# Kernel tuning notes

Measured on AMD Instinct MI355X. Metric: run time of the kernel, lower is better.

## Reference

```python
import jax, jax.numpy as jnp
import numpy as np

B, S, D, H = 32, 577, 768, 12
DH = D // H
MLP = 4 * D
EPS = 1e-5


def _layernorm(x, g, b):
    m = jnp.mean(x, axis=-1, keepdims=True)
    v = jnp.mean((x - m) ** 2, axis=-1, keepdims=True)
    return (x - m) * jax.lax.rsqrt(v + EPS) * g + b


def setup_inputs() -> dict:
    key = jax.random.key(0)
    ks = jax.random.split(key, 12)
    w = lambda k, shp: (jax.random.normal(k, shp, dtype=jnp.float32) * 0.02)
    return {
        "x": jax.random.normal(ks[0], (B, S, D), dtype=jnp.float32),
        "ln1_g": jnp.ones((D,), jnp.float32), "ln1_b": jnp.zeros((D,), jnp.float32),
        "ln2_g": jnp.ones((D,), jnp.float32), "ln2_b": jnp.zeros((D,), jnp.float32),
        "wq": w(ks[1], (H, DH, DH)), "bq": jnp.zeros((H, DH), jnp.float32),
        "wk": w(ks[2], (H, DH, DH)), "bk": jnp.zeros((H, DH), jnp.float32),
        "wv": w(ks[3], (H, DH, DH)), "bv": jnp.zeros((H, DH), jnp.float32),
        "w1": w(ks[4], (D, MLP)), "b1": jnp.zeros((MLP,), jnp.float32),
        "w2": w(ks[5], (MLP, D)), "b2": jnp.zeros((D,), jnp.float32),
    }


def reference(x, ln1_g, ln1_b, ln2_g, ln2_b, wq, bq, wk, bk, wv, bv, w1, b1, w2, b2):
    b, s, d = x.shape
    xn = _layernorm(x, ln1_g, ln1_b)
    xh = xn.reshape(b, s, H, DH)  # split heads along last dim (as in torch slicing)
    # per-head linear maps, batched over heads: [B,H,S,DH]
    q = jnp.einsum('bshd,hdo->bhso', xh, wq) + bq[:, None, :]
    k = jnp.einsum('bshd,hdo->bhso', xh, wk) + bk[:, None, :]
    v = jnp.einsum('bshd,hdo->bhso', xh, wv) + bv[:, None, :]
    scores = jnp.einsum('bhso,bhto->bhst', q, k) / (DH ** 0.5)
    attn = jax.nn.softmax(scores, axis=-1)  # softmax over keys (torch dim=1 of [S,S])
    o = jnp.einsum('bhst,bhtd->bshd', attn, v).reshape(b, s, d)
    out = x + o
    yn = _layernorm(out, ln2_g, ln2_b)
    h = jax.nn.gelu(yn @ w1 + b1, approximate=False)  # torch GELU default is erf-based
    return out + h @ w2 + b2
```

## Files before the change

kernel.cpp:

```cpp
#include <hip/hip_runtime.h>

#define S_LEN 577
#define SPAD  640
#define DMODEL 768
#define NH 12
#define DHEAD 64
#define MLPD 3072
#define NROWS (32 * 577)
#define MPAD  18688
#define NBH   (32 * 12)
#define LOG2E 1.44269504088896340736f

typedef __attribute__((ext_vector_type(8))) short s8v;
typedef __attribute__((ext_vector_type(4))) float f4v;

#define MFMA16(a, b, c) __builtin_amdgcn_mfma_f32_16x16x32_bf16((a), (b), (c), 0, 0, 0)

__device__ __forceinline__ short f2bf(float f) {
  union { float f; unsigned u; } a; a.f = f;
  unsigned r = a.u + 0x7FFFu + ((a.u >> 16) & 1u);
  return (short)(r >> 16);
}
__device__ __forceinline__ short f2bfF(float f) {
  union { float f; unsigned u; } a; a.f = f;
  return (short)((a.u + 0x8000u) >> 16);
}

__device__ __forceinline__ void gload16(const short* g, const short* l) {
  __builtin_amdgcn_global_load_lds(
      (const __attribute__((address_space(1))) void*)g,
      (__attribute__((address_space(3))) void*)l, 16, 0, 0);
}

__global__ __launch_bounds__(256) void transpose_w(const float* __restrict__ in,
                                                   short* __restrict__ out, int R, int C) {
  __shared__ float tile[32][33];
  int c0 = blockIdx.x * 32, r0 = blockIdx.y * 32;
  int tx = threadIdx.x, ty = threadIdx.y;
  for (int i = ty; i < 32; i += 8) tile[i][tx] = in[(size_t)(r0 + i) * C + c0 + tx];
  __syncthreads();
  for (int i = ty; i < 32; i += 8) out[(size_t)(c0 + i) * R + r0 + tx] = f2bf(tile[tx][i]);
}

__global__ __launch_bounds__(256) void prep_qkv(const float* __restrict__ wq, const float* __restrict__ wk,
                                                const float* __restrict__ wv, short* __restrict__ oq,
                                                short* __restrict__ ok, short* __restrict__ ov) {
  int h = blockIdx.x, t = threadIdx.x;
  const float* src0 = wq + (size_t)h * 4096;
  const float* src1 = wk + (size_t)h * 4096;
  const float* src2 = wv + (size_t)h * 4096;
  short* dst0 = oq + (size_t)h * 4096;
  short* dst1 = ok + (size_t)h * 4096;
  short* dst2 = ov + (size_t)h * 4096;
  for (int i = t; i < 4096; i += 256) {
    int o = i >> 6, d = i & 63;
    dst0[i] = f2bf(src0[d * 64 + o]);
    dst1[i] = f2bf(src1[d * 64 + o]);
    dst2[i] = f2bf(src2[d * 64 + o]);
  }
}

__global__ __launch_bounds__(256) void pad_kv(short* __restrict__ kg, short* __restrict__ vt) {
  int idx = blockIdx.x * 256 + threadIdx.x;
  const int padw = SPAD - S_LEN;
  const int per = DHEAD * padw;
  if (idx >= NBH * per) return;
  int bh = idx / per, r = idx - bh * per;
  int col = r / padw, s = S_LEN + (r - col * padw);
  vt[((size_t)bh * DHEAD + col) * SPAD + s] = 0;
  kg[((size_t)bh * SPAD + s) * DHEAD + col] = 0;
}

__global__ __launch_bounds__(256) void ln_kernel(const float* __restrict__ x, const float* __restrict__ g,
                                                 const float* __restrict__ bta, short* __restrict__ out) {
  int row = blockIdx.x;
  int t = threadIdx.x;
  const float* xr = x + (size_t)row * DMODEL;
  float v0 = xr[t], v1 = xr[t + 256], v2 = xr[t + 512];
  float s = v0 + v1 + v2;
  float s2 = v0 * v0 + v1 * v1 + v2 * v2;
  for (int o = 32; o; o >>= 1) { s += __shfl_down(s, o); s2 += __shfl_down(s2, o); }
  __shared__ float red[8];
  if ((t & 63) == 0) { int w = t >> 6; red[w] = s; red[4 + w] = s2; }
  __syncthreads();
  s = red[0] + red[1] + red[2] + red[3];
  s2 = red[4] + red[5] + red[6] + red[7];
  float m = s * (1.f / DMODEL);
  float rs = rsqrtf(s2 * (1.f / DMODEL) - m * m + 1e-5f);
  short* orow = out + (size_t)row * DMODEL;
  orow[t]       = f2bf((v0 - m) * rs * g[t]       + bta[t]);
  orow[t + 256] = f2bf((v1 - m) * rs * g[t + 256] + bta[t + 256]);
  orow[t + 512] = f2bf((v2 - m) * rs * g[t + 512] + bta[t + 512]);
}

__global__ __launch_bounds__(256) void qkv_kernel(const short* __restrict__ xn,
    const short* __restrict__ wqt, const short* __restrict__ wkt, const short* __restrict__ wvt,
    const float* __restrict__ bq, const float* __restrict__ bk, const float* __restrict__ bv,
    short* __restrict__ qg, short* __restrict__ kg, short* __restrict__ vt) {
  __shared__ __align__(16) short wl[3][64][72];
  int bid = blockIdx.x;
  int h = bid % NH, mt = bid / NH;
  int t = threadIdx.x;
  {
    int o = t >> 2, d0 = (t & 3) * 16;
    const short* s0 = wqt + (size_t)h * 4096 + o * 64 + d0;
    const short* s1 = wkt + (size_t)h * 4096 + o * 64 + d0;
    const short* s2 = wvt + (size_t)h * 4096 + o * 64 + d0;
    *(uint4*)&wl[0][o][d0]     = *(const uint4*)s0;
    *(uint4*)&wl[0][o][d0 + 8] = *(const uint4*)(s0 + 8);
    *(uint4*)&wl[1][o][d0]     = *(const uint4*)s1;
    *(uint4*)&wl[1][o][d0 + 8] = *(const uint4*)(s1 + 8);
    *(uint4*)&wl[2][o][d0]     = *(const uint4*)s2;
    *(uint4*)&wl[2][o][d0 + 8] = *(const uint4*)(s2 + 8);
  }
  __syncthreads();
  int w = t >> 6, l = t & 63, l15 = l & 15, lh = l >> 4;
  int m0 = mt * 64 + w * 16;
  if (m0 >= NROWS) return;
  f4v z = {0.f, 0.f, 0.f, 0.f};
  f4v aq[4], ak[4], av[4];
#pragma unroll
  for (int nt = 0; nt < 4; ++nt) { aq[nt] = z; ak[nt] = z; av[nt] = z; }
  const short* xrow = xn + (size_t)(m0 + l15) * DMODEL + h * DHEAD;
#pragma unroll
  for (int kk = 0; kk < 64; kk += 32) {
    s8v af = *(const s8v*)(xrow + kk + lh * 8);
#pragma unroll
    for (int nt = 0; nt < 4; ++nt) {
      s8v b0 = *(const s8v*)&wl[0][nt * 16 + l15][kk + lh * 8];
      s8v b1 = *(const s8v*)&wl[1][nt * 16 + l15][kk + lh * 8];
      s8v b2 = *(const s8v*)&wl[2][nt * 16 + l15][kk + lh * 8];
      aq[nt] = MFMA16(af, b0, aq[nt]);
      ak[nt] = MFMA16(af, b1, ak[nt]);
      av[nt] = MFMA16(af, b2, av[nt]);
    }
  }
#pragma unroll
  for (int nt = 0; nt < 4; ++nt) {
    int col = nt * 16 + l15;
    float biq = bq[h * DHEAD + col], bik = bk[h * DHEAD + col], biv = bv[h * DHEAD + col];
#pragma unroll
    for (int i = 0; i < 4; ++i) {
      int m = m0 + lh * 4 + i;
      int bb = m / S_LEN;
      int ss = m - bb * S_LEN;
      int bh = bb * NH + h;
      qg[((size_t)bh * S_LEN + ss) * DHEAD + col] = f2bf((aq[nt][i] + biq) * (0.125f * LOG2E));
      kg[((size_t)bh * SPAD + ss) * DHEAD + col]  = f2bf(ak[nt][i] + bik);
      vt[((size_t)bh * DHEAD + col) * SPAD + ss]  = f2bf(av[nt][i] + biv);
    }
  }
}

__global__ __launch_bounds__(64, 2) void attn_kernel(const short* __restrict__ qg, const short* __restrict__ kg,
                                                     const short* __restrict__ vt, const float* __restrict__ x,
                                                     float* __restrict__ outp) {
  __shared__ __align__(16) short Pb[2][64][72];
  int bh = blockIdx.x;
  int qt = blockIdx.y;
  int h = bh % NH, b = bh / NH;
  int l = threadIdx.x & 63, l15 = l & 15, lh = l >> 4;
  int q0 = qt * 64;
  size_t qbase = (size_t)bh * S_LEN * DHEAD;
  size_t kbase = (size_t)bh * SPAD * DHEAD;
  size_t vbase = (size_t)bh * DHEAD * SPAD;
  s8v aq[4][2];
#pragma unroll
  for (int f = 0; f < 4; ++f) {
    int qrow = q0 + f * 16 + l15; if (qrow > 576) qrow = 576;
    const short* qp = qg + qbase + (size_t)qrow * DHEAD + lh * 8;
    aq[f][0] = *(const s8v*)qp;
    aq[f][1] = *(const s8v*)(qp + 32);
  }
  f4v z = {0.f, 0.f, 0.f, 0.f};
  f4v z16 = {-16.f, -16.f, -16.f, -16.f};
  f4v acc[4][4];
  float lsum[4][4];
#pragma unroll
  for (int f = 0; f < 4; ++f) {
#pragma unroll
    for (int dt = 0; dt < 4; ++dt) acc[f][dt] = z;
#pragma unroll
    for (int i = 0; i < 4; ++i) lsum[f][i] = 0.f;
  }

  s8v kf0[4], kf1[4], vf[2][4];
  f4v sc[2][4];

#define LOADK(KB)                                                      \
  {                                                                    \
    _Pragma("unroll")                                                  \
    for (int nt = 0; nt < 4; ++nt) {                                   \
      const short* kp = kg + kbase + (size_t)((KB) + nt * 16 + l15) * DHEAD + lh * 8; \
      kf0[nt] = *(const s8v*)kp;                                       \
      kf1[nt] = *(const s8v*)(kp + 32);                                \
    }                                                                  \
  }

#define LOADV(KB)                                                      \
  {                                                                    \
    _Pragma("unroll")                                                  \
    for (int kk2 = 0; kk2 < 2; ++kk2) {                                \
      const short* vp = vt + vbase + (KB) + kk2 * 32 + lh * 8;         \
      _Pragma("unroll")                                                \
      for (int dt = 0; dt < 4; ++dt)                                   \
        vf[kk2][dt] = *(const s8v*)(vp + (size_t)(dt * 16 + l15) * SPAD); \
    }                                                                  \
  }

#define QKT_H(FH)                                                      \
  {                                                                    \
    __builtin_amdgcn_s_setprio(1);                                     \
    _Pragma("unroll")                                                  \
    for (int nt = 0; nt < 4; ++nt) {                                   \
      _Pragma("unroll")                                                \
      for (int fo = 0; fo < 2; ++fo) {                                 \
        f4v a = MFMA16(aq[2 * (FH) + fo][0], kf0[nt], z16);            \
        a = MFMA16(aq[2 * (FH) + fo][1], kf1[nt], a);                  \
        sc[fo][nt] = a;                                                \
      }                                                                \
    }                                                                  \
    __builtin_amdgcn_s_setprio(0);                                     \
  }

#define SMAX_H(FH, PAR, MASK)                                          \
  {                                                                    \
    if (MASK) {                                                        \
      _Pragma("unroll")                                                \
      for (int nt = 0; nt < 4; ++nt) {                                 \
        int col = 576 + nt * 16 + l15;                                 \
        if (col > 576) {                                               \
          _Pragma("unroll")                                            \
          for (int fo = 0; fo < 2; ++fo) {                             \
            sc[fo][nt][0] = sc[fo][nt][1] = sc[fo][nt][2] = sc[fo][nt][3] = -1e30f; } \
        }                                                              \
      }                                                                \
    }                                                                  \
    _Pragma("unroll")                                                  \
    for (int fo = 0; fo < 2; ++fo)                                     \
      _Pragma("unroll")                                                \
      for (int i = 0; i < 4; ++i) {                                    \
        float s = lsum[2 * (FH) + fo][i];                              \
        _Pragma("unroll")                                              \
        for (int nt = 0; nt < 4; ++nt) {                               \
          float e = exp2f(sc[fo][nt][i]);                              \
          s += e;                                                      \
          Pb[PAR][(2 * (FH) + fo) * 16 + lh * 4 + i][nt * 16 + l15] = f2bfF(e); \
        }                                                              \
        lsum[2 * (FH) + fo][i] = s;                                    \
      }                                                                \
  }

#define PVT(PAR)                                                       \
  {                                                                    \
    __builtin_amdgcn_s_setprio(1);                                     \
    _Pragma("unroll")                                                  \
    for (int kk2 = 0; kk2 < 2; ++kk2) {                                \
      _Pragma("unroll")                                                \
      for (int f = 0; f < 4; ++f) {                                    \
        s8v af = *(const s8v*)&Pb[PAR][f * 16 + l15][kk2 * 32 + lh * 8]; \
        _Pragma("unroll")                                              \
        for (int dt = 0; dt < 4; ++dt)                                 \
          acc[f][dt] = MFMA16(af, vf[kk2][dt], acc[f][dt]);            \
      }                                                                \
    }                                                                  \
    __builtin_amdgcn_s_setprio(0);                                     \
  }

  LOADK(0);
  QKT_H(0);
  SMAX_H(0, 0, false);
  QKT_H(1);
  LOADK(64);
  SMAX_H(1, 0, false);

  for (int kt = 0; kt < 10; ++kt) {
    int par = kt & 1;
    LOADV(kt * 64);
    if (kt < 9) {
      bool mask = (kt == 8);
      QKT_H(0);
      SMAX_H(0, par ^ 1, mask);
      QKT_H(1);
      if (kt < 8) LOADK((kt + 2) * 64);
      SMAX_H(1, par ^ 1, mask);
    }
    PVT(par);
  }
#undef LOADK
#undef LOADV
#undef QKT_H
#undef SMAX_H
#undef PVT
#pragma unroll
  for (int f = 0; f < 4; ++f)
#pragma unroll
    for (int i = 0; i < 4; ++i) {
      float s = lsum[f][i];
      s += __shfl_xor(s, 1);
      s += __shfl_xor(s, 2);
      s += __shfl_xor(s, 4);
      s += __shfl_xor(s, 8);
      int srow = q0 + f * 16 + lh * 4 + i;
      if (srow > 576) continue;
      float inv = __builtin_amdgcn_rcpf(s);
      size_t idx0 = ((size_t)b * S_LEN + srow) * DMODEL + h * DHEAD + l15;
#pragma unroll
      for (int dt = 0; dt < 4; ++dt) {
        size_t idx = idx0 + dt * 16;
        outp[idx] = x[idx] + acc[f][dt][i] * inv;
      }
    }
}

#define BARR asm volatile("s_barrier" ::: "memory")

#define STAGE_HALF(G, SH, bufi, half, ktile)                                       \
  do {                                                                             \
    _Pragma("unroll") for (int rd = 0; rd < 2; ++rd) {                             \
      int rw_ = rd * 64 + (tid >> 3);                                              \
      int sl_ = (tid & 7) ^ (rw_ & 7);                                             \
      gload16((G) + (size_t)((half) * 128 + rw_) * K + (ktile) * 64 + sl_ * 8,     \
              &SH[bufi][(half) * 128 + rw_][(tid & 7) * 8]);                       \
    }                                                                              \
  } while (0)

#define READ_A(rh)                                                                 \
  _Pragma("unroll") for (int mt = 0; mt < 4; ++mt)                                 \
    _Pragma("unroll") for (int kh = 0; kh < 2; ++kh)                               \
      af[mt][kh] = *(const s8v*)&sA[cur][(rh) * 128 + wr * 64 + mt * 16 + l15]     \
                                    [((kh * 4 + lh) ^ s7) * 8];

#define READ_B(BF, chh)                                                            \
  _Pragma("unroll") for (int nt = 0; nt < 2; ++nt)                                 \
    _Pragma("unroll") for (int kh = 0; kh < 2; ++kh)                               \
      BF[nt][kh] = *(const s8v*)&sB[cur][wc * 64 + (chh) * 32 + nt * 16 + l15]     \
                                    [((kh * 4 + lh) ^ s7) * 8];

#define DO_MFMA(rh, ch, BF)                                                        \
  __builtin_amdgcn_s_setprio(1);                                                   \
  _Pragma("unroll") for (int mt = 0; mt < 4; ++mt)                                 \
    _Pragma("unroll") for (int nt = 0; nt < 2; ++nt)                               \
      _Pragma("unroll") for (int kh = 0; kh < 2; ++kh)                             \
        acc[(rh) * 4 + mt][(ch) * 2 + nt] =                                        \
            MFMA16(af[mt][kh], BF[nt][kh], acc[(rh) * 4 + mt][(ch) * 2 + nt]);     \
  __builtin_amdgcn_s_setprio(0);

#define GEMM8_BODY                                                                 \
  int nwg = gridDim.x;                                                             \
  int orig = blockIdx.x;                                                           \
  int qq = nwg >> 3, rr = nwg & 7;                                                 \
  int xcd = orig & 7, lin = orig >> 3;                                             \
  int wg = (xcd < rr ? xcd * (qq + 1) : rr * (qq + 1) + (xcd - rr) * qq) + lin;    \
  int nx = N >> 8;                                                                 \
  int n0 = (wg % nx) * 256, m0 = (wg / nx) * 256;                                  \
  int tid = threadIdx.x;                                                           \
  int wid = tid >> 6, l = tid & 63, l15 = l & 15, lh = l >> 4;                     \
  int s7 = l15 & 7;                                                                \
  int wr = wid >> 2, wc = wid & 3;                                                 \
  const short* Ab = A + (size_t)m0 * K;                                            \
  const short* Bb = Bt + (size_t)n0 * K;                                           \
  f4v z = {0.f, 0.f, 0.f, 0.f};                                                    \
  f4v acc[8][4];                                                                   \
  _Pragma("unroll") for (int i = 0; i < 8; ++i)                                    \
    _Pragma("unroll") for (int j = 0; j < 4; ++j) acc[i][j] = z;                   \
  s8v af[4][2], bf0[2][2], bf1[2][2];                                              \
  int NT = K >> 6;                                                                 \
  STAGE_HALF(Ab, sA, 0, 0, 0); STAGE_HALF(Ab, sA, 0, 1, 0);                        \
  STAGE_HALF(Bb, sB, 0, 0, 0); STAGE_HALF(Bb, sB, 0, 1, 0);                        \
  STAGE_HALF(Ab, sA, 1, 0, 1); STAGE_HALF(Bb, sB, 1, 0, 1);                        \
  STAGE_HALF(Bb, sB, 1, 1, 1);                                                     \
  asm volatile("s_waitcnt vmcnt(6)" ::: "memory");                                 \
  BARR;                                                                            \
  int cur = 0;                                                                     \
  for (int kt = 0; kt < NT; ++kt) {                                                \
    int nxt = cur ^ 1;                                                             \
    READ_A(0); READ_B(bf0, 0);                                                     \
    if (kt + 1 < NT) STAGE_HALF(Ab, sA, nxt, 1, kt + 1);                           \
    BARR; DO_MFMA(0, 0, bf0); BARR;                                                \
    READ_B(bf1, 1);                                                                \
    if (kt + 2 < NT) STAGE_HALF(Ab, sA, cur, 0, kt + 2);                           \
    BARR; DO_MFMA(0, 1, bf1); BARR;                                                \
    READ_A(1);                                                                     \
    if (kt + 2 < NT) STAGE_HALF(Bb, sB, cur, 0, kt + 2);                           \
    BARR; DO_MFMA(1, 1, bf1); BARR;                                                \
    if (kt + 2 < NT) STAGE_HALF(Bb, sB, cur, 1, kt + 2);                           \
    BARR; DO_MFMA(1, 0, bf0);                                                      \
    if (kt < NT - 2)       { asm volatile("s_waitcnt vmcnt(6)" ::: "memory"); }    \
    else if (kt == NT - 2) { asm volatile("s_waitcnt vmcnt(0)" ::: "memory"); }    \
    BARR;                                                                          \
    cur = nxt;                                                                     \
  }

__global__ __launch_bounds__(512, 1) void gemm_gelu(const short* __restrict__ A, const short* __restrict__ Bt,
                                                    const float* __restrict__ bias, short* __restrict__ C,
                                                    int M, int N, int K) {
  __shared__ __align__(16) short sA[2][256][64];
  __shared__ __align__(16) short sB[2][256][64];
  GEMM8_BODY
#pragma unroll
  for (int ri = 0; ri < 8; ++ri)
#pragma unroll
    for (int ci = 0; ci < 4; ++ci) {
      int col = n0 + wc * 64 + (ci >> 1) * 32 + (ci & 1) * 16 + l15;
      float bi = bias[col];
#pragma unroll
      for (int i = 0; i < 4; ++i) {
        int row = m0 + (ri >> 2) * 128 + wr * 64 + (ri & 3) * 16 + lh * 4 + i;
        float v = acc[ri][ci][i] + bi;
        float u = v * (2.30221838f + 0.10294364f * v * v);
        v = v * __builtin_amdgcn_rcpf(1.f + exp2f(-u));
        C[(size_t)row * N + col] = f2bfF(v);
      }
    }
}

__global__ __launch_bounds__(512, 1) void gemm_res(const short* __restrict__ A, const short* __restrict__ Bt,
                                                   const float* __restrict__ bias, float* __restrict__ outp,
                                                   int Mvalid, int N, int K) {
  __shared__ __align__(16) short sA[2][256][64];
  __shared__ __align__(16) short sB[2][256][64];
  GEMM8_BODY
#pragma unroll
  for (int ri = 0; ri < 8; ++ri)
#pragma unroll
    for (int ci = 0; ci < 4; ++ci) {
      int col = n0 + wc * 64 + (ci >> 1) * 32 + (ci & 1) * 16 + l15;
      float bi = bias[col];
#pragma unroll
      for (int i = 0; i < 4; ++i) {
        int row = m0 + (ri >> 2) * 128 + wr * 64 + (ri & 3) * 16 + lh * 4 + i;
        if (row < Mvalid) {
          size_t idx = (size_t)row * N + col;
          outp[idx] += acc[ri][ci][i] + bi;
        }
      }
    }
}

extern "C" void kernel_launch(void* const* d_in, const int* in_sizes, int n_in,
                              void* d_out, int out_size, void* d_ws, size_t ws_size,
                              hipStream_t stream) {
  const float* x    = (const float*)d_in[0];
  const float* ln1g = (const float*)d_in[1];
  const float* ln1b = (const float*)d_in[2];
  const float* ln2g = (const float*)d_in[3];
  const float* ln2b = (const float*)d_in[4];
  const float* wq   = (const float*)d_in[5];
  const float* bq   = (const float*)d_in[6];
  const float* wk   = (const float*)d_in[7];
  const float* bk   = (const float*)d_in[8];
  const float* wv   = (const float*)d_in[9];
  const float* bv   = (const float*)d_in[10];
  const float* w1   = (const float*)d_in[11];
  const float* b1   = (const float*)d_in[12];
  const float* w2   = (const float*)d_in[13];
  const float* b2   = (const float*)d_in[14];
  float* outp = (float*)d_out;

  char* ws = (char*)d_ws;
  size_t off = 0;
  auto carve = [&](size_t elems) -> short* {
    short* p = (short*)(ws + off);
    off += elems * sizeof(short);
    off = (off + 255) & ~(size_t)255;
    return p;
  };
  short* yn   = carve((size_t)MPAD * DMODEL);
  short* w1t  = carve((size_t)MLPD * DMODEL);
  short* w2t  = carve((size_t)DMODEL * MLPD);
  short* wqt  = carve((size_t)NH * 64 * 64);
  short* wkt  = carve((size_t)NH * 64 * 64);
  short* wvt  = carve((size_t)NH * 64 * 64);
  size_t union_base = off;
  short* hbuf = carve((size_t)MPAD * MLPD);
  off = union_base;
  short* xn   = carve((size_t)NROWS * DMODEL);
  short* qg   = carve((size_t)NBH * S_LEN * DHEAD);
  short* kg   = carve((size_t)NBH * SPAD * DHEAD);
  short* vtb  = carve((size_t)NBH * DHEAD * SPAD);
  (void)ws_size; (void)in_sizes; (void)n_in; (void)out_size;

  transpose_w<<<dim3(MLPD / 32, DMODEL / 32), dim3(32, 8), 0, stream>>>(w1, w1t, DMODEL, MLPD);
  transpose_w<<<dim3(DMODEL / 32, MLPD / 32), dim3(32, 8), 0, stream>>>(w2, w2t, MLPD, DMODEL);
  prep_qkv<<<NH, 256, 0, stream>>>(wq, wk, wv, wqt, wkt, wvt);
  pad_kv<<<(NBH * DHEAD * (SPAD - S_LEN) + 255) / 256, 256, 0, stream>>>(kg, vtb);

  ln_kernel<<<NROWS, 256, 0, stream>>>(x, ln1g, ln1b, xn);

  qkv_kernel<<<((NROWS + 63) / 64) * NH, 256, 0, stream>>>(xn, wqt, wkt, wvt, bq, bk, bv, qg, kg, vtb);

  attn_kernel<<<dim3(NBH, 10), 64, 0, stream>>>(qg, kg, vtb, x, outp);

  ln_kernel<<<NROWS, 256, 0, stream>>>(outp, ln2g, ln2b, yn);

  gemm_gelu<<<dim3((MPAD / 256) * (MLPD / 256)), 512, 0, stream>>>(yn, w1t, b1, hbuf, MPAD, MLPD, DMODEL);
  gemm_res<<<dim3((MPAD / 256) * (DMODEL / 256)), 512, 0, stream>>>(hbuf, w2t, b2, outp, NROWS, DMODEL, MLPD);
}
```

Baseline: 452.5 us.

## Replace ping-pong 8-wave MLP GEMM with 16-wave BK=32 double-buffered GEMM

Rewrites the shared GEMM body for both MLP kernels. The old version was an 8-wave, 256x256-tile ping-pong schedule with K-tiles of 64 and hand-placed barriers and vmcnt waits. The new version uses 1024 threads (16 waves, each owning a 64x64 sub-tile), K-tiles of 32, a simple LDS double buffer with one __syncthreads per K step, and a new XOR swizzle. This makes the synchronisation simpler and doubles the number of waves. In exchange it loses the fine-grained overlap of loads with MFMA, adds more barriers per unit of work, and relies on implicit waits for the async LDS loads.

```diff
diff --git a/kernel.cpp b/kernel.cpp
--- a/kernel.cpp
+++ b/kernel.cpp
@@ -313,40 +313,7 @@
     }
 }
 
-#define BARR asm volatile("s_barrier" ::: "memory")
-
-#define STAGE_HALF(G, SH, bufi, half, ktile)                                       \
-  do {                                                                             \
-    _Pragma("unroll") for (int rd = 0; rd < 2; ++rd) {                             \
-      int rw_ = rd * 64 + (tid >> 3);                                              \
-      int sl_ = (tid & 7) ^ (rw_ & 7);                                             \
-      gload16((G) + (size_t)((half) * 128 + rw_) * K + (ktile) * 64 + sl_ * 8,     \
-              &SH[bufi][(half) * 128 + rw_][(tid & 7) * 8]);                       \
-    }                                                                              \
-  } while (0)
-
-#define READ_A(rh)                                                                 \
-  _Pragma("unroll") for (int mt = 0; mt < 4; ++mt)                                 \
-    _Pragma("unroll") for (int kh = 0; kh < 2; ++kh)                               \
-      af[mt][kh] = *(const s8v*)&sA[cur][(rh) * 128 + wr * 64 + mt * 16 + l15]     \
-                                    [((kh * 4 + lh) ^ s7) * 8];
-
-#define READ_B(BF, chh)                                                            \
-  _Pragma("unroll") for (int nt = 0; nt < 2; ++nt)                                 \
-    _Pragma("unroll") for (int kh = 0; kh < 2; ++kh)                               \
-      BF[nt][kh] = *(const s8v*)&sB[cur][wc * 64 + (chh) * 32 + nt * 16 + l15]     \
-                                    [((kh * 4 + lh) ^ s7) * 8];
-
-#define DO_MFMA(rh, ch, BF)                                                        \
-  __builtin_amdgcn_s_setprio(1);                                                   \
-  _Pragma("unroll") for (int mt = 0; mt < 4; ++mt)                                 \
-    _Pragma("unroll") for (int nt = 0; nt < 2; ++nt)                               \
-      _Pragma("unroll") for (int kh = 0; kh < 2; ++kh)                             \
-        acc[(rh) * 4 + mt][(ch) * 2 + nt] =                                        \
-            MFMA16(af[mt][kh], BF[nt][kh], acc[(rh) * 4 + mt][(ch) * 2 + nt]);     \
-  __builtin_amdgcn_s_setprio(0);
-
-#define GEMM8_BODY                                                                 \
+#define GEMM32_BODY                                                                \
   int nwg = gridDim.x;                                                             \
   int orig = blockIdx.x;                                                           \
   int qq = nwg >> 3, rr = nwg & 7;                                                 \
@@ -356,58 +323,58 @@
   int n0 = (wg % nx) * 256, m0 = (wg / nx) * 256;                                  \
   int tid = threadIdx.x;                                                           \
   int wid = tid >> 6, l = tid & 63, l15 = l & 15, lh = l >> 4;                     \
-  int s7 = l15 & 7;                                                                \
   int wr = wid >> 2, wc = wid & 3;                                                 \
+  int srow = tid >> 2, sslot = tid & 3;                                            \
+  int scol = (sslot ^ ((srow >> 1) & 3)) * 8;                                      \
   const short* Ab = A + (size_t)m0 * K;                                            \
   const short* Bb = Bt + (size_t)n0 * K;                                           \
   f4v z = {0.f, 0.f, 0.f, 0.f};                                                    \
-  f4v acc[8][4];                                                                   \
-  _Pragma("unroll") for (int i = 0; i < 8; ++i)                                    \
+  f4v acc[4][4];                                                                   \
+  _Pragma("unroll") for (int i = 0; i < 4; ++i)                                    \
     _Pragma("unroll") for (int j = 0; j < 4; ++j) acc[i][j] = z;                   \
-  s8v af[4][2], bf0[2][2], bf1[2][2];                                              \
-  int NT = K >> 6;                                                                 \
-  STAGE_HALF(Ab, sA, 0, 0, 0); STAGE_HALF(Ab, sA, 0, 1, 0);                        \
-  STAGE_HALF(Bb, sB, 0, 0, 0); STAGE_HALF(Bb, sB, 0, 1, 0);                        \
-  STAGE_HALF(Ab, sA, 1, 0, 1); STAGE_HALF(Bb, sB, 1, 0, 1);                        \
-  STAGE_HALF(Bb, sB, 1, 1, 1);                                                     \
-  asm volatile("s_waitcnt vmcnt(6)" ::: "memory");                                 \
-  BARR;                                                                            \
+  s8v af[4], bf[4];                                                                \
+  int NT = K >> 5;                                                                 \
+  gload16(Ab + (size_t)srow * K + scol, &sA[0][srow][sslot * 8]);                  \
+  gload16(Bb + (size_t)srow * K + scol, &sB[0][srow][sslot * 8]);                  \
   int cur = 0;                                                                     \
   for (int kt = 0; kt < NT; ++kt) {                                                \
-    int nxt = cur ^ 1;                                                             \
-    READ_A(0); READ_B(bf0, 0);                                                     \
-    if (kt + 1 < NT) STAGE_HALF(Ab, sA, nxt, 1, kt + 1);                           \
-    BARR; DO_MFMA(0, 0, bf0); BARR;                                                \
-    READ_B(bf1, 1);                                                                \
-    if (kt + 2 < NT) STAGE_HALF(Ab, sA, cur, 0, kt + 2);                           \
-    BARR; DO_MFMA(0, 1, bf1); BARR;                                                \
-    READ_A(1);                                                                     \
-    if (kt + 2 < NT) STAGE_HALF(Bb, sB, cur, 0, kt + 2);                           \
-    BARR; DO_MFMA(1, 1, bf1); BARR;                                                \
-    if (kt + 2 < NT) STAGE_HALF(Bb, sB, cur, 1, kt + 2);                           \
-    BARR; DO_MFMA(1, 0, bf0);                                                      \
-    if (kt < NT - 2)       { asm volatile("s_waitcnt vmcnt(6)" ::: "memory"); }    \
-    else if (kt == NT - 2) { asm volatile("s_waitcnt vmcnt(0)" ::: "memory"); }    \
-    BARR;                                                                          \
-    cur = nxt;                                                                     \
-  }
-
-__global__ __launch_bounds__(512, 1) void gemm_gelu(const short* __restrict__ A, const short* __restrict__ Bt,
-                                                    const float* __restrict__ bias, short* __restrict__ C,
-                                                    int M, int N, int K) {
-  __shared__ __align__(16) short sA[2][256][64];
-  __shared__ __align__(16) short sB[2][256][64];
-  GEMM8_BODY
-#pragma unroll
-  for (int ri = 0; ri < 8; ++ri)
-#pragma unroll
-    for (int ci = 0; ci < 4; ++ci) {
-      int col = n0 + wc * 64 + (ci >> 1) * 32 + (ci & 1) * 16 + l15;
+    __syncthreads();                                                               \
+    if (kt + 1 < NT) {                                                             \
+      gload16(Ab + (size_t)srow * K + (kt + 1) * 32 + scol, &sA[cur ^ 1][srow][sslot * 8]); \
+      gload16(Bb + (size_t)srow * K + (kt + 1) * 32 + scol, &sB[cur ^ 1][srow][sslot * 8]); \
+    }                                                                              \
+    _Pragma("unroll") for (int mt = 0; mt < 4; ++mt) {                             \
+      int r_ = wr * 64 + mt * 16 + l15;                                            \
+      af[mt] = *(const s8v*)&sA[cur][r_][(lh ^ ((r_ >> 1) & 3)) * 8];              \
+    }                                                                              \
+    _Pragma("unroll") for (int nt2 = 0; nt2 < 4; ++nt2) {                          \
+      int r_ = wc * 64 + nt2 * 16 + l15;                                           \
+      bf[nt2] = *(const s8v*)&sB[cur][r_][(lh ^ ((r_ >> 1) & 3)) * 8];             \
+    }                                                                              \
+    __builtin_amdgcn_s_setprio(1);                                                 \
+    _Pragma("unroll") for (int mt = 0; mt < 4; ++mt)                               \
+      _Pragma("unroll") for (int nt2 = 0; nt2 < 4; ++nt2)                          \
+        acc[mt][nt2] = MFMA16(af[mt], bf[nt2], acc[mt][nt2]);                      \
+    __builtin_amdgcn_s_setprio(0);                                                 \
+    cur ^= 1;                                                                      \
+  }
+
+__global__ __launch_bounds__(1024) void gemm_gelu(const short* __restrict__ A, const short* __restrict__ Bt,
+                                                  const float* __restrict__ bias, short* __restrict__ C,
+                                                  int M, int N, int K) {
+  __shared__ __align__(16) short sA[2][256][32];
+  __shared__ __align__(16) short sB[2][256][32];
+  GEMM32_BODY
+#pragma unroll
+  for (int mt = 0; mt < 4; ++mt)
+#pragma unroll
+    for (int nt2 = 0; nt2 < 4; ++nt2) {
+      int col = n0 + wc * 64 + nt2 * 16 + l15;
       float bi = bias[col];
 #pragma unroll
       for (int i = 0; i < 4; ++i) {
-        int row = m0 + (ri >> 2) * 128 + wr * 64 + (ri & 3) * 16 + lh * 4 + i;
-        float v = acc[ri][ci][i] + bi;
+        int row = m0 + wr * 64 + mt * 16 + lh * 4 + i;
+        float v = acc[mt][nt2][i] + bi;
         float u = v * (2.30221838f + 0.10294364f * v * v);
         v = v * __builtin_amdgcn_rcpf(1.f + exp2f(-u));
         C[(size_t)row * N + col] = f2bfF(v);
@@ -415,24 +382,24 @@
     }
 }
 
-__global__ __launch_bounds__(512, 1) void gemm_res(const short* __restrict__ A, const short* __restrict__ Bt,
-                                                   const float* __restrict__ bias, float* __restrict__ outp,
-                                                   int Mvalid, int N, int K) {
-  __shared__ __align__(16) short sA[2][256][64];
-  __shared__ __align__(16) short sB[2][256][64];
-  GEMM8_BODY
-#pragma unroll
-  for (int ri = 0; ri < 8; ++ri)
-#pragma unroll
-    for (int ci = 0; ci < 4; ++ci) {
-      int col = n0 + wc * 64 + (ci >> 1) * 32 + (ci & 1) * 16 + l15;
+__global__ __launch_bounds__(1024) void gemm_res(const short* __restrict__ A, const short* __restrict__ Bt,
+                                                 const float* __restrict__ bias, float* __restrict__ outp,
+                                                 int Mvalid, int N, int K) {
+  __shared__ __align__(16) short sA[2][256][32];
+  __shared__ __align__(16) short sB[2][256][32];
+  GEMM32_BODY
+#pragma unroll
+  for (int mt = 0; mt < 4; ++mt)
+#pragma unroll
+    for (int nt2 = 0; nt2 < 4; ++nt2) {
+      int col = n0 + wc * 64 + nt2 * 16 + l15;
       float bi = bias[col];
 #pragma unroll
       for (int i = 0; i < 4; ++i) {
-        int row = m0 + (ri >> 2) * 128 + wr * 64 + (ri & 3) * 16 + lh * 4 + i;
+        int row = m0 + wr * 64 + mt * 16 + lh * 4 + i;
         if (row < Mvalid) {
           size_t idx = (size_t)row * N + col;
-          outp[idx] += acc[ri][ci][i] + bi;
+          outp[idx] += acc[mt][nt2][i] + bi;
         }
       }
     }
@@ -494,6 +461,6 @@
 
   ln_kernel<<<NROWS, 256, 0, stream>>>(outp, ln2g, ln2b, yn);
 
-  gemm_gelu<<<dim3((MPAD / 256) * (MLPD / 256)), 512, 0, stream>>>(yn, w1t, b1, hbuf, MPAD, MLPD, DMODEL);
-  gemm_res<<<dim3((MPAD / 256) * (DMODEL / 256)), 512, 0, stream>>>(hbuf, w2t, b2, outp, NROWS, DMODEL, MLPD);
-}
+  gemm_gelu<<<dim3((MPAD / 256) * (MLPD / 256)), 1024, 0, stream>>>(yn, w1t, b1, hbuf, MPAD, MLPD, DMODEL);
+  gemm_res<<<dim3((MPAD / 256) * (DMODEL / 256)), 1024, 0, stream>>>(hbuf, w2t, b2, outp, NROWS, DMODEL, MLPD);
+}
```

New measurement: 448.4 us. About the same (-0.9%).
